# Performance work log

Measured on AMD Instinct MI355X. Metric: run time of the kernel, lower is better.

## Reference

```python
import jax, jax.numpy as jnp
import numpy as np

B = 32768
IN_F = 256
OUT_F = 256


def setup_inputs() -> dict:
    key = jax.random.key(0)
    k1, k2 = jax.random.split(key)
    x = jax.random.normal(k1, (B, IN_F, 4), dtype=jnp.float32)
    std = 1.0 / np.sqrt(4 * IN_F)
    weight = jax.random.normal(k2, (OUT_F, IN_F, 4), dtype=jnp.float32) * std
    weight = weight.at[..., 0].add(0.5)  # quaternion Xavier: bias real part
    bias = jnp.zeros((OUT_F, 4), dtype=jnp.float32)
    return {"x": x, "weight": weight, "bias": bias}


def _quat_linear(x, weight, bias):
    # x: (..., in, 4) with components (w, x, y, z); weight: (out, in, 4)
    # Hamilton product q1=W, q2=x, summed over in -> 16 structured matmuls.
    xw, xx, xy, xz = x[..., 0], x[..., 1], x[..., 2], x[..., 3]
    ww, wx, wy, wz = weight[..., 0], weight[..., 1], weight[..., 2], weight[..., 3]

    def mm(w, v):  # (out, in) x (..., in) -> (..., out)
        return jnp.einsum('oi,...i->...o', w, v)

    yw = mm(ww, xw) - mm(wx, xx) - mm(wy, xy) - mm(wz, xz)
    yx = mm(ww, xx) + mm(wx, xw) + mm(wy, xz) - mm(wz, xy)
    yy = mm(ww, xy) - mm(wx, xz) + mm(wy, xw) + mm(wz, xx)
    yz = mm(ww, xz) + mm(wx, xy) - mm(wy, xx) + mm(wz, xw)

    y = jnp.stack([yw, yx, yy, yz], axis=-1)  # (..., out, 4)
    return y + bias


def reference(x, weight, bias):
    return _quat_linear(x, weight, bias)
```

## Files before the change

kernel.cpp:

```cpp
#include <hip/hip_runtime.h>


typedef __bf16 bf16x8_t __attribute__((ext_vector_type(8)));
typedef short short8    __attribute__((ext_vector_type(8)));
typedef float f32x4     __attribute__((ext_vector_type(4)));
typedef float f32x8     __attribute__((ext_vector_type(8)));

typedef const unsigned int __attribute__((address_space(1)))* gas_uint_ptr;
typedef unsigned int __attribute__((address_space(3)))*       las_uint_ptr;

__global__ __launch_bounds__(256) void build_weff(const float* __restrict__ w,
                                                  unsigned short* __restrict__ wq) {
    int idx = blockIdx.x * 256 + threadIdx.x;
    int n = idx >> 10, k = idx & 1023;
    int o = n >> 2, r = n & 3, i = k >> 2, c = k & 3;
    int s = r ^ c;
    float v = w[o * 1024 + i * 4 + s];
    if ((0x284E >> (r * 4 + c)) & 1) v = -v;
    __bf16 b = (__bf16)v;
    union { __bf16 b; unsigned short u; } cv;
    cv.b = b;
    wq[idx] = cv.u;
}

__global__ __launch_bounds__(256) void qlin_gemm(const float* __restrict__ X,
                                                 const unsigned short* __restrict__ Wq,
                                                 const float* __restrict__ bias,
                                                 float* __restrict__ out) {
    __shared__ __align__(16) unsigned short As[128 * 64];
    __shared__ __align__(16) unsigned short Bs[128 * 64];

    const int t    = threadIdx.x;
    const int w    = t >> 6;
    const int l    = t & 63;
    const int lo16 = l & 15;
    const int hi2  = l >> 4;
    const int m0   = (blockIdx.x >> 3) * 128;
    const int n0   = (blockIdx.x & 7) * 128;
    const int wm   = (w & 1) * 64;
    const int wn   = (w >> 1) * 64;

    f32x4 acc[4][4] = {};

    for (int kt = 0; kt < 16; ++kt) {
        const int k0 = kt * 64;
        __syncthreads();

#pragma unroll
        for (int jj = 0; jj < 4; ++jj) {
            const int c16  = jj * 256 + t;
            const int row  = c16 >> 3;
            const int kcol = (c16 & 7) * 8;
            const unsigned short* gp = Wq + (n0 + row) * 1024 + k0 + kcol;
            __builtin_amdgcn_global_load_lds((gas_uint_ptr)gp,
                                             (las_uint_ptr)(Bs + c16 * 8),
                                             16, 0, 0);
        }

#pragma unroll
        for (int jj = 0; jj < 4; ++jj) {
            const int c16  = jj * 256 + t;
            const int row  = c16 >> 3;
            const int kcol = (c16 & 7) * 8;
            const float* gp = X + (m0 + row) * 1024 + k0 + kcol;
            f32x4 lo = *(const f32x4*)gp;
            f32x4 hi = *(const f32x4*)(gp + 4);
            f32x8 f8 = __builtin_shufflevector(lo, hi, 0, 1, 2, 3, 4, 5, 6, 7);
            bf16x8_t bv = __builtin_convertvector(f8, bf16x8_t);
            union { bf16x8_t b; short8 s; } cv;
            cv.b = bv;
            *(short8*)(As + c16 * 8) = cv.s;
        }

        __syncthreads();

#pragma unroll
        for (int ks = 0; ks < 2; ++ks) {
            short8 af[4], bf[4];
#pragma unroll
            for (int mt = 0; mt < 4; ++mt)
                af[mt] = *(const short8*)(As + (wm + mt * 16 + lo16) * 64 + ks * 32 + hi2 * 8);
#pragma unroll
            for (int nt = 0; nt < 4; ++nt)
                bf[nt] = *(const short8*)(Bs + (wn + nt * 16 + lo16) * 64 + ks * 32 + hi2 * 8);
#pragma unroll
            for (int mt = 0; mt < 4; ++mt)
#pragma unroll
                for (int nt = 0; nt < 4; ++nt)
                    acc[mt][nt] = __builtin_amdgcn_mfma_f32_16x16x32_bf16(
                        af[mt], bf[nt], acc[mt][nt], 0, 0, 0);
        }
    }

#pragma unroll
    for (int nt = 0; nt < 4; ++nt) {
        const int n  = n0 + wn + nt * 16 + lo16;
        const float bv = bias[n];
#pragma unroll
        for (int mt = 0; mt < 4; ++mt) {
            const int mb = m0 + wm + mt * 16 + hi2 * 4;
#pragma unroll
            for (int r = 0; r < 4; ++r)
                out[(mb + r) * 1024 + n] = acc[mt][nt][r] + bv;
        }
    }
}

extern "C" void kernel_launch(void* const* d_in, const int* in_sizes, int n_in,
                              void* d_out, int out_size, void* d_ws, size_t ws_size,
                              hipStream_t stream) {
    const float* x  = (const float*)d_in[0];
    const float* wt = (const float*)d_in[1];
    const float* bs = (const float*)d_in[2];
    float* out = (float*)d_out;
    unsigned short* wq = (unsigned short*)d_ws;

    build_weff<<<4096, 256, 0, stream>>>(wt, wq);
    qlin_gemm<<<2048, 256, 0, stream>>>(x, wq, bs, out);

    (void)in_sizes; (void)n_in; (void)out_size; (void)ws_size;
}
```

Before: 346.0 us.

## XOR-swizzle LDS tiles and remap block indices for XCD locality

```diff
diff --git a/kernel.cpp b/kernel.cpp
--- a/kernel.cpp
+++ b/kernel.cpp
@@ -35,8 +35,13 @@
     const int l    = t & 63;
     const int lo16 = l & 15;
     const int hi2  = l >> 4;
-    const int m0   = (blockIdx.x >> 3) * 128;
-    const int n0   = (blockIdx.x & 7) * 128;
+
+    const int bid  = blockIdx.x;
+    const int xcd  = bid & 7;
+    const int s    = bid >> 3;
+    const int m0   = (xcd * 32 + (s >> 3)) * 128;
+    const int n0   = (s & 7) * 128;
+
     const int wm   = (w & 1) * 64;
     const int wn   = (w >> 1) * 64;
 
@@ -48,41 +53,47 @@
 
 #pragma unroll
         for (int jj = 0; jj < 4; ++jj) {
-            const int c16  = jj * 256 + t;
-            const int row  = c16 >> 3;
-            const int kcol = (c16 & 7) * 8;
-            const unsigned short* gp = Wq + (n0 + row) * 1024 + k0 + kcol;
+            const int p    = jj * 256 + t;
+            const int row  = p >> 3;
+            const int g    = (p & 7) ^ (row & 7);
+            const unsigned short* gp = Wq + (n0 + row) * 1024 + k0 + g * 8;
             __builtin_amdgcn_global_load_lds((gas_uint_ptr)gp,
-                                             (las_uint_ptr)(Bs + c16 * 8),
+                                             (las_uint_ptr)(Bs + p * 8),
                                              16, 0, 0);
         }
 
 #pragma unroll
         for (int jj = 0; jj < 4; ++jj) {
-            const int c16  = jj * 256 + t;
-            const int row  = c16 >> 3;
-            const int kcol = (c16 & 7) * 8;
-            const float* gp = X + (m0 + row) * 1024 + k0 + kcol;
+            const int c    = jj * 256 + t;
+            const int row  = c >> 3;
+            const int g    = c & 7;
+            const float* gp = X + (m0 + row) * 1024 + k0 + g * 8;
             f32x4 lo = *(const f32x4*)gp;
             f32x4 hi = *(const f32x4*)(gp + 4);
             f32x8 f8 = __builtin_shufflevector(lo, hi, 0, 1, 2, 3, 4, 5, 6, 7);
             bf16x8_t bv = __builtin_convertvector(f8, bf16x8_t);
             union { bf16x8_t b; short8 s; } cv;
             cv.b = bv;
-            *(short8*)(As + c16 * 8) = cv.s;
+            const int p = row * 8 + (g ^ (row & 7));
+            *(short8*)(As + p * 8) = cv.s;
         }
 
         __syncthreads();
 
 #pragma unroll
         for (int ks = 0; ks < 2; ++ks) {
+            const int g = ks * 4 + hi2;
             short8 af[4], bf[4];
 #pragma unroll
-            for (int mt = 0; mt < 4; ++mt)
-                af[mt] = *(const short8*)(As + (wm + mt * 16 + lo16) * 64 + ks * 32 + hi2 * 8);
+            for (int mt = 0; mt < 4; ++mt) {
+                const int r = wm + mt * 16 + lo16;
+                af[mt] = *(const short8*)(As + (r * 8 + (g ^ (r & 7))) * 8);
+            }
 #pragma unroll
-            for (int nt = 0; nt < 4; ++nt)
-                bf[nt] = *(const short8*)(Bs + (wn + nt * 16 + lo16) * 64 + ks * 32 + hi2 * 8);
+            for (int nt = 0; nt < 4; ++nt) {
+                const int r = wn + nt * 16 + lo16;
+                bf[nt] = *(const short8*)(Bs + (r * 8 + (g ^ (r & 7))) * 8);
+            }
 #pragma unroll
             for (int mt = 0; mt < 4; ++mt)
 #pragma unroll
```

Result: no change. 340.2 us (-1.7%).
